# Kernel tuning notes

Hardware: AMD Instinct MI355X
Metric: run time of the kernel (lower is better)

Reference implementation:

```python
import jax, jax.numpy as jnp
import numpy as np

DIM = 2560
N_HEAD = 32
HEAD_DIM = 80
ROT_DIM = 32  # head_dim * partial_rotary_factor
INTER = 10240
EPS = 1e-5
BASE = 10000.0


def setup_inputs() -> dict:
    key = jax.random.key(0)
    ks = jax.random.split(key, 12)
    B, S, D, I = 1, 2048, DIM, INTER
    s = lambda k, shape, scale: (jax.random.normal(k, shape, jnp.float32) * scale)
    return {
        "x": s(ks[0], (B, S, D), 1.0),
        "input_pos": jnp.arange(S, dtype=jnp.int32),
        "mask": jnp.tril(jnp.ones((S, S), dtype=bool)),
        "ln_w": jnp.ones((D,), jnp.float32),
        "ln_b": jnp.zeros((D,), jnp.float32),
        "wqkv_w": s(ks[1], (3 * D, D), 0.02),
        "wqkv_b": jnp.zeros((3 * D,), jnp.float32),
        "wo_w": s(ks[2], (D, D), 0.02),
        "wo_b": jnp.zeros((D,), jnp.float32),
        "w1_w": s(ks[3], (I, D), 0.02),
        "w1_b": jnp.zeros((I,), jnp.float32),
        "w2_w": s(ks[4], (D, I), 0.02),
        "w2_b": jnp.zeros((D,), jnp.float32),
    }


def _rope_cos_sin(positions):
    # positions: [S] int; returns cos,sin of shape [S, ROT_DIM]
    inv_freq = 1.0 / (BASE ** (jnp.arange(0, ROT_DIM, 2, dtype=jnp.float32) / ROT_DIM))
    freqs = positions.astype(jnp.float32)[:, None] * inv_freq[None, :]  # [S, ROT/2]
    emb = jnp.concatenate([freqs, freqs], axis=-1)  # [S, ROT]
    return jnp.cos(emb), jnp.sin(emb)


def _rotate_half(t):
    t1, t2 = jnp.split(t, 2, axis=-1)
    return jnp.concatenate([-t2, t1], axis=-1)


def _apply_rope(t, cos, sin):
    # t: [B,H,S,hd]; rotary applied to first ROT_DIM dims (partial rotary)
    t_rot, t_pass = t[..., :ROT_DIM], t[..., ROT_DIM:]
    t_rot = t_rot * cos[None, None] + _rotate_half(t_rot) * sin[None, None]
    return jnp.concatenate([t_rot, t_pass], axis=-1)


def reference(x, input_pos, mask, ln_w, ln_b, wqkv_w, wqkv_b, wo_w, wo_b,
              w1_w, w1_b, w2_w, w2_b):
    B, S, D = x.shape
    H, hd = N_HEAD, HEAD_DIM
    # shared LayerNorm (parallel block)
    mu = jnp.mean(x, axis=-1, keepdims=True)
    var = jnp.mean(jnp.square(x - mu), axis=-1, keepdims=True)
    h = (x - mu) * jax.lax.rsqrt(var + EPS) * ln_w + ln_b

    # fused QKV
    qkv = h @ wqkv_w.T + wqkv_b  # [B,S,3D]
    q, k, v = jnp.split(qkv, 3, axis=-1)
    q = q.reshape(B, S, H, hd).transpose(0, 2, 1, 3)  # [B,H,S,hd]
    k = k.reshape(B, S, H, hd).transpose(0, 2, 1, 3)
    v = v.reshape(B, S, H, hd).transpose(0, 2, 1, 3)

    cos, sin = _rope_cos_sin(input_pos)
    q = _apply_rope(q, cos, sin)
    k = _apply_rope(k, cos, sin)

    # causal attention
    scores = jnp.einsum("bhqd,bhkd->bhqk", q, k) / np.sqrt(hd).astype(np.float32)
    scores = jnp.where(mask[None, None], scores, jnp.float32(-1e9))
    attn = jax.nn.softmax(scores, axis=-1)
    y = jnp.einsum("bhqk,bhkd->bhqd", attn, v)  # [B,H,S,hd]
    y = y.transpose(0, 2, 1, 3).reshape(B, S, D)
    attn_out = y @ wo_w.T + wo_b

    # fused MLP (phi2: gelu_new / tanh approx)
    ffn = jax.nn.gelu(h @ w1_w.T + w1_b, approximate=True) @ w2_w.T + w2_b

    return attn_out + ffn + x
```

## Files before the change

kernel.cpp:

```cpp
#include <hip/hip_runtime.h>
#include <cstdint>

#define S_LEN 2048
#define DMODEL 2560
#define NHEADS 32
#define HDIM 80
#define DINTER 10240

typedef unsigned short u16;
typedef __bf16 bf16x8 __attribute__((ext_vector_type(8)));
typedef float f32x4 __attribute__((ext_vector_type(4)));

__device__ __forceinline__ float us2f(u16 u) {
  return __builtin_bit_cast(float, ((uint32_t)u) << 16);
}
__device__ __forceinline__ u16 f2us(float f) {
  uint32_t x = __builtin_bit_cast(uint32_t, f);
  x += 0x7fffu + ((x >> 16) & 1u);
  return (u16)(x >> 16);
}

typedef __attribute__((address_space(1))) void gas_void;
typedef __attribute__((address_space(3))) void las_void;
__device__ __forceinline__ void gld16(const void* g, void* l) {
  __builtin_amdgcn_global_load_lds((gas_void*)g, (las_void*)l, 16, 0, 0);
}

#define VMW(N) asm volatile("s_waitcnt vmcnt(" #N ")" ::: "memory")
#define BARRIER()                          \
  do {                                     \
    asm volatile("" ::: "memory");         \
    __builtin_amdgcn_s_barrier();          \
    asm volatile("" ::: "memory");         \
  } while (0)

__global__ void f2b_kernel(const float* __restrict__ src, u16* __restrict__ dst) {
  const size_t i = ((size_t)blockIdx.x * 256 + threadIdx.x) * 8;
  const float4 a = *(const float4*)(src + i);
  const float4 b = *(const float4*)(src + i + 4);
  u16 o[8] = {f2us(a.x), f2us(a.y), f2us(a.z), f2us(a.w),
              f2us(b.x), f2us(b.y), f2us(b.z), f2us(b.w)};
  *(uint4*)(dst + i) = *(uint4*)o;
}

__global__ void initout_kernel(const float* __restrict__ x,
                               const float* __restrict__ wo_b,
                               const float* __restrict__ w2_b,
                               float* __restrict__ out) {
  const size_t idx = ((size_t)blockIdx.x * 256 + threadIdx.x) * 4;
  const int c0 = (int)(idx % DMODEL);
  const float4 vx = *(const float4*)(x + idx);
  const float4 b1 = *(const float4*)(wo_b + c0);
  const float4 b2 = *(const float4*)(w2_b + c0);
  float4 vo;
  vo.x = vx.x + b1.x + b2.x;
  vo.y = vx.y + b1.y + b2.y;
  vo.z = vx.z + b1.z + b2.z;
  vo.w = vx.w + b1.w + b2.w;
  *(float4*)(out + idx) = vo;
}

__global__ void ln_kernel(const float* __restrict__ x, const float* __restrict__ w,
                          const float* __restrict__ b, u16* __restrict__ h) {
  const int s = blockIdx.x, tid = threadIdx.x;
  const float* xr = x + (size_t)s * DMODEL;
  float v[10];
  float sum = 0.f, sq = 0.f;
#pragma unroll
  for (int j = 0; j < 10; j++) {
    v[j] = xr[tid + j * 256];
    sum += v[j];
    sq += v[j] * v[j];
  }
#pragma unroll
  for (int o = 32; o > 0; o >>= 1) {
    sum += __shfl_down(sum, o, 64);
    sq += __shfl_down(sq, o, 64);
  }
  __shared__ float red[8];
  const int wave = tid >> 6, lane = tid & 63;
  if (lane == 0) { red[wave] = sum; red[4 + wave] = sq; }
  __syncthreads();
  sum = red[0] + red[1] + red[2] + red[3];
  sq = red[4] + red[5] + red[6] + red[7];
  const float mu = sum * (1.0f / DMODEL);
  const float var = sq * (1.0f / DMODEL) - mu * mu;
  const float rstd = rsqrtf(var + 1e-5f);
  u16* hr = h + (size_t)s * DMODEL;
#pragma unroll
  for (int j = 0; j < 10; j++) {
    const int d = tid + j * 256;
    hr[d] = f2us((v[j] - mu) * rstd * w[d] + b[d]);
  }
}

template <int ACT, int MODE>
__launch_bounds__(512, 2)
__global__ void gemm256(const u16* __restrict__ A, const u16* __restrict__ B,
                        const float* __restrict__ bias, void* __restrict__ Cv,
                        int M, int N, int K) {
  __shared__ __align__(16) u16 lds[3][16384];
  const int tid = threadIdx.x;
  const int w = tid >> 6, lane = tid & 63;
  const int quad = lane >> 4, l15 = lane & 15;
  const int wm = w >> 2, wn = w & 3;

  const int nwg = gridDim.x * gridDim.y;
  const int flat = blockIdx.x + gridDim.x * blockIdx.y;
  const int swz = (flat & 7) * (nwg >> 3) + (flat >> 3);
  const int ntN = N >> 8;
  const int bm = swz / ntN, bn = swz % ntN;

  const int Kc = K / gridDim.z;
  const int k0 = Kc * blockIdx.z;
  const int nt = Kc >> 5;

  const int g = ((lane & 3) ^ ((lane >> 3) & 3)) * 8;
  const u16* Ag = A + ((size_t)bm * 256 + w * 32 + (lane >> 2)) * K + k0 + g;
  const u16* Bg = B + ((size_t)bn * 256 + w * 32 + (lane >> 2)) * K + k0 + g;
  const size_t k16 = (size_t)16 * K;
  const int aw = w * 1024;

  const int rswz = (quad ^ ((l15 >> 1) & 3)) * 8;
  const int arow = wm * 128 + l15;
  const int brow = wn * 64 + l15;

#define STG(T)                                                               \
  do {                                                                       \
    const int q_ = (T) % 3;                                                  \
    const size_t ko_ = (size_t)(T) * 32;                                     \
    gld16(Ag + ko_, &lds[q_][aw]);                                           \
    gld16(Ag + ko_ + k16, &lds[q_][aw + 512]);                               \
    gld16(Bg + ko_, &lds[q_][8192 + aw]);                                    \
    gld16(Bg + ko_ + k16, &lds[q_][8192 + aw + 512]);                        \
  } while (0)

#define TILE_BODY(T)                                                         \
  do {                                                                       \
    const int qb_ = (T) % 3;                                                 \
    bf16x8 aF[8], bF[4];                                                     \
    _Pragma("unroll") for (int mf_ = 0; mf_ < 8; mf_++)                      \
        aF[mf_] = *(const bf16x8*)&lds[qb_][(arow + mf_ * 16) * 32 + rswz];  \
    _Pragma("unroll") for (int nf_ = 0; nf_ < 4; nf_++)                      \
        bF[nf_] = *(const bf16x8*)&lds[qb_][8192 + (brow + nf_ * 16) * 32 + rswz]; \
    __builtin_amdgcn_s_setprio(1);                                           \
    _Pragma("unroll") for (int mf_ = 0; mf_ < 8; mf_++)                      \
    _Pragma("unroll") for (int nf_ = 0; nf_ < 4; nf_++)                      \
        acc[mf_][nf_] = __builtin_amdgcn_mfma_f32_16x16x32_bf16(             \
            aF[mf_], bF[nf_], acc[mf_][nf_], 0, 0, 0);                       \
    __builtin_amdgcn_s_setprio(0);                                           \
  } while (0)

  f32x4 acc[8][4] = {};

  STG(0);
  STG(1);

  for (int t = 0; t < nt - 1; ++t) {
    VMW(4);
    BARRIER();
    if (t + 2 < nt) STG(t + 2);
    TILE_BODY(t);
  }
  {
    VMW(0);
    BARRIER();
    TILE_BODY(nt - 1);
  }

#pragma unroll
  for (int nf = 0; nf < 4; nf++) {
    const int col = bn * 256 + wn * 64 + nf * 16 + l15;
    const float bv = (MODE == 0) ? bias[col] : 0.f;
#pragma unroll
    for (int mf = 0; mf < 8; mf++) {
      const int row0 = bm * 256 + wm * 128 + mf * 16 + quad * 4;
#pragma unroll
      for (int r = 0; r < 4; r++) {
        float v = acc[mf][nf][r] + bv;
        if (ACT == 1) {
          const float tt = v * (0.7978845608f + 0.0356774081f * v * v);
          v = 0.5f * v * (1.0f + tanhf(tt));
        }
        if (MODE == 0)
          ((u16*)Cv)[(size_t)(row0 + r) * N + col] = f2us(v);
        else
          atomicAdd((float*)Cv + (size_t)(row0 + r) * N + col, v);
      }
    }
  }
#undef STG
#undef TILE_BODY
}

__global__ void rope_kernel(u16* __restrict__ qkv, const int* __restrict__ pos) {
  const int idx = blockIdx.x * 256 + threadIdx.x;
  const int i = idx & 15;
  const int which = (idx >> 4) & 1;
  const int hh = (idx >> 5) & 31;
  const int s = idx >> 10;
  const float p = (float)pos[s];
  const float freq = p * expf(-0.57564627324851f * (float)i);
  float sn, c;
  sincosf(freq, &sn, &c);
  u16* base = qkv + (size_t)s * (3 * DMODEL) + which * DMODEL + hh * HDIM + i;
  const float t0 = us2f(base[0]), t1 = us2f(base[16]);
  base[0] = f2us(t0 * c - t1 * sn);
  base[16] = f2us(t1 * c + t0 * sn);
}

__global__ void attn_kernel(const u16* __restrict__ qkv, u16* __restrict__ y) {
  const int qt = (int)gridDim.x - 1 - (int)blockIdx.x;
  const int h = blockIdx.y;
  const int tid = threadIdx.x, wave = tid >> 6, lane = tid & 63;
  const int quad = lane >> 4, l15 = lane & 15;
  const int qbase = qt * 64;

  __shared__ __align__(16) u16 Qs[64 * 104];
  __shared__ __align__(16) u16 Ks[2][64 * 104];
  __shared__ __align__(16) u16 Vts[2][80 * 88];
  __shared__ __align__(16) u16 Ps[4][2][16 * 40];

  if (tid < 128) {
    const int b = tid >> 6, r = tid & 63;
    u16* z = &Ks[b][r * 104 + 80];
    *(uint4*)z = uint4{0, 0, 0, 0};
    *(uint4*)(z + 8) = uint4{0, 0, 0, 0};
  } else if (tid < 192) {
    const int r = tid & 63;
    u16* z = &Qs[r * 104 + 80];
    *(uint4*)z = uint4{0, 0, 0, 0};
    *(uint4*)(z + 8) = uint4{0, 0, 0, 0};
    *(uint4*)(z + 16) = uint4{0, 0, 0, 0};
  }

  {
    const int r = tid >> 2, c = tid & 3;
    const u16* src = qkv + (size_t)(qbase + r) * (3 * DMODEL) + h * HDIM + c * 20;
    u16* dst = Qs + r * 104 + c * 20;
#pragma unroll
    for (int j = 0; j < 5; j++) {
      ushort4 uv = *(const ushort4*)(src + j * 4);
      ushort4 ov;
      ov.x = f2us(us2f(uv.x) * 0.11180339887f);
      ov.y = f2us(us2f(uv.y) * 0.11180339887f);
      ov.z = f2us(us2f(uv.z) * 0.11180339887f);
      ov.w = f2us(us2f(uv.w) * 0.11180339887f);
      *(ushort4*)(dst + j * 4) = ov;
    }
  }

  {
    const int r = tid >> 2, c4 = (tid & 3) * 20;
    const u16* sK = qkv + (size_t)r * (3 * DMODEL) + DMODEL + h * HDIM + c4;
    u16* dK = &Ks[0][r * 104 + c4];
#pragma unroll
    for (int j = 0; j < 5; j++) *(uint2*)(dK + j * 4) = *(const uint2*)(sK + j * 4);
  }
  if (tid < 160) {
    const int p = tid & 31, cc = tid >> 5;
    const u16* sV = qkv + (size_t)(2 * p) * (3 * DMODEL) + 2 * DMODEL + h * HDIM + cc * 16;
    const uint4 a0 = *(const uint4*)sV;
    const uint4 b0 = *(const uint4*)(sV + 8);
    const uint4 a1 = *(const uint4*)(sV + 3 * DMODEL);
    const uint4 b1 = *(const uint4*)(sV + 3 * DMODEL + 8);
    const uint32_t A0[8] = {a0.x, a0.y, a0.z, a0.w, b0.x, b0.y, b0.z, b0.w};
    const uint32_t A1[8] = {a1.x, a1.y, a1.z, a1.w, b1.x, b1.y, b1.z, b1.w};
    uint32_t* dV = (uint32_t*)Vts[0];
#pragma unroll
    for (int d = 0; d < 16; d++) {
      const int j = d >> 1, s = (d & 1) * 16;
      const uint32_t o = ((A0[j] >> s) & 0xffffu) | (((A1[j] >> s) & 0xffffu) << 16);
      dV[(cc * 16 + d) * 44 + p] = o;
    }
  }

  float m_i[4], l_i[4];
  f32x4 oacc[5] = {};
#pragma unroll
  for (int r = 0; r < 4; r++) { m_i[r] = -1e30f; l_i[r] = 0.f; }

  __syncthreads();

  bf16x8 aq[3];
#pragma unroll
  for (int ks = 0; ks < 3; ks++)
    aq[ks] = *(const bf16x8*)&Qs[(wave * 16 + l15) * 104 + ks * 32 + quad * 8];

  const int n_iter = qt + 1;
  uint2 kr[5];
  uint4 v0a = {}, v0b = {}, v1a = {}, v1b = {};

  for (int it = 0; it < n_iter; ++it) {
    const int cur = it & 1;
    const bool more = (it + 1 < n_iter);
    if (more) {
      const int kcn = (it + 1) * 64;
      const int r = tid >> 2, c4 = (tid & 3) * 20;
      const u16* sK = qkv + (size_t)(kcn + r) * (3 * DMODEL) + DMODEL + h * HDIM + c4;
#pragma unroll
      for (int j = 0; j < 5; j++) kr[j] = *(const uint2*)(sK + j * 4);
      if (tid < 160) {
        const int p = tid & 31, cc = tid >> 5;
        const u16* sV =
            qkv + (size_t)(kcn + 2 * p) * (3 * DMODEL) + 2 * DMODEL + h * HDIM + cc * 16;
        v0a = *(const uint4*)sV;
        v0b = *(const uint4*)(sV + 8);
        v1a = *(const uint4*)(sV + 3 * DMODEL);
        v1b = *(const uint4*)(sV + 3 * DMODEL + 8);
      }
    }

    const int kc0 = it * 64;
    f32x4 st[4] = {};
#pragma unroll
    for (int ks = 0; ks < 3; ks++)
#pragma unroll
      for (int t = 0; t < 4; t++) {
        bf16x8 bk = *(const bf16x8*)&Ks[cur][(t * 16 + l15) * 104 + ks * 32 + quad * 8];
        st[t] = __builtin_amdgcn_mfma_f32_16x16x32_bf16(aq[ks], bk, st[t], 0, 0, 0);
      }

    float sv[4][4], mx[4];
    if (it == qt) {
#pragma unroll
      for (int r = 0; r < 4; r++) {
        const int qr = qbase + wave * 16 + quad * 4 + r;
#pragma unroll
        for (int t = 0; t < 4; t++) {
          const int kc = kc0 + t * 16 + l15;
          sv[t][r] = (kc <= qr) ? st[t][r] : -1e30f;
        }
      }
    } else {
#pragma unroll
      for (int r = 0; r < 4; r++)
#pragma unroll
        for (int t = 0; t < 4; t++) sv[t][r] = st[t][r];
    }
#pragma unroll
    for (int r = 0; r < 4; r++)
      mx[r] = fmaxf(fmaxf(sv[0][r], sv[1][r]), fmaxf(sv[2][r], sv[3][r]));
#pragma unroll
    for (int o = 1; o < 16; o <<= 1)
#pragma unroll
      for (int r = 0; r < 4; r++) mx[r] = fmaxf(mx[r], __shfl_xor(mx[r], o, 64));

    float alpha[4], rs[4];
#pragma unroll
    for (int r = 0; r < 4; r++) {
      const float mnew = fmaxf(m_i[r], mx[r]);
      alpha[r] = __expf(m_i[r] - mnew);
      m_i[r] = mnew;
      const float p0 = __expf(sv[0][r] - mnew);
      const float p1 = __expf(sv[1][r] - mnew);
      const float p2 = __expf(sv[2][r] - mnew);
      const float p3 = __expf(sv[3][r] - mnew);
      rs[r] = (p0 + p1) + (p2 + p3);
      const int ro = (quad * 4 + r) * 40;
      Ps[wave][0][ro + l15] = f2us(p0);
      Ps[wave][0][ro + 16 + l15] = f2us(p1);
      Ps[wave][1][ro + l15] = f2us(p2);
      Ps[wave][1][ro + 16 + l15] = f2us(p3);
    }
#pragma unroll
    for (int o = 1; o < 16; o <<= 1)
#pragma unroll
      for (int r = 0; r < 4; r++) rs[r] += __shfl_xor(rs[r], o, 64);
#pragma unroll
    for (int r = 0; r < 4; r++) l_i[r] = l_i[r] * alpha[r] + rs[r];
#pragma unroll
    for (int dt = 0; dt < 5; dt++)
#pragma unroll
      for (int r = 0; r < 4; r++) oacc[dt][r] *= alpha[r];

    bf16x8 pf0 = *(const bf16x8*)&Ps[wave][0][l15 * 40 + quad * 8];
    bf16x8 pf1 = *(const bf16x8*)&Ps[wave][1][l15 * 40 + quad * 8];
#pragma unroll
    for (int dt = 0; dt < 5; dt++) {
      bf16x8 vf0 = *(const bf16x8*)&Vts[cur][(dt * 16 + l15) * 88 + quad * 8];
      bf16x8 vf1 = *(const bf16x8*)&Vts[cur][(dt * 16 + l15) * 88 + 32 + quad * 8];
      oacc[dt] = __builtin_amdgcn_mfma_f32_16x16x32_bf16(pf0, vf0, oacc[dt], 0, 0, 0);
      oacc[dt] = __builtin_amdgcn_mfma_f32_16x16x32_bf16(pf1, vf1, oacc[dt], 0, 0, 0);
    }

    if (more) {
      const int r = tid >> 2, c4 = (tid & 3) * 20;
      u16* dK = &Ks[cur ^ 1][r * 104 + c4];
#pragma unroll
      for (int j = 0; j < 5; j++) *(uint2*)(dK + j * 4) = kr[j];
      if (tid < 160) {
        const int p = tid & 31, cc = tid >> 5;
        const uint32_t A0[8] = {v0a.x, v0a.y, v0a.z, v0a.w,
                                v0b.x, v0b.y, v0b.z, v0b.w};
        const uint32_t A1[8] = {v1a.x, v1a.y, v1a.z, v1a.w,
                                v1b.x, v1b.y, v1b.z, v1b.w};
        uint32_t* dV = (uint32_t*)Vts[cur ^ 1];
#pragma unroll
        for (int d = 0; d < 16; d++) {
          const int j = d >> 1, s = (d & 1) * 16;
          const uint32_t o =
              ((A0[j] >> s) & 0xffffu) | (((A1[j] >> s) & 0xffffu) << 16);
          dV[(cc * 16 + d) * 44 + p] = o;
        }
      }
    }
    __syncthreads();
  }

#pragma unroll
  for (int dt = 0; dt < 5; dt++)
#pragma unroll
    for (int r = 0; r < 4; r++) {
      const int row = qbase + wave * 16 + quad * 4 + r;
      y[(size_t)row * DMODEL + h * HDIM + dt * 16 + l15] = f2us(oacc[dt][r] / l_i[r]);
    }
}

extern "C" void kernel_launch(void* const* d_in, const int* in_sizes, int n_in,
                              void* d_out, int out_size, void* d_ws, size_t ws_size,
                              hipStream_t stream) {
  const float* x = (const float*)d_in[0];
  const int* pos = (const int*)d_in[1];
  const float* ln_w = (const float*)d_in[3];
  const float* ln_b = (const float*)d_in[4];
  const float* wqkv_w = (const float*)d_in[5];
  const float* wqkv_b = (const float*)d_in[6];
  const float* wo_w = (const float*)d_in[7];
  const float* wo_b = (const float*)d_in[8];
  const float* w1_w = (const float*)d_in[9];
  const float* w1_b = (const float*)d_in[10];
  const float* w2_w = (const float*)d_in[11];
  const float* w2_b = (const float*)d_in[12];
  float* out = (float*)d_out;

  char* ws = (char*)d_ws;
  u16* wbuf = (u16*)(ws);
  u16* h = (u16*)(ws + 52428800);
  u16* ffn1 = (u16*)(ws + 62914560);
  u16* qkv = (u16*)(ws + 62914560);
  u16* yAtt = (u16*)(ws + 94371840);

  ln_kernel<<<S_LEN, 256, 0, stream>>>(x, ln_w, ln_b, h);
  initout_kernel<<<(S_LEN * DMODEL / 4) / 256, 256, 0, stream>>>(x, wo_b, w2_b, out);

  f2b_kernel<<<(DINTER * DMODEL) / 2048, 256, 0, stream>>>(w1_w, wbuf);
  gemm256<1, 0><<<dim3(DINTER / 256, S_LEN / 256, 1), 512, 0, stream>>>(
      h, wbuf, w1_b, ffn1, S_LEN, DINTER, DMODEL);
  f2b_kernel<<<(DMODEL * DINTER) / 2048, 256, 0, stream>>>(w2_w, wbuf);
  gemm256<0, 2><<<dim3(DMODEL / 256, S_LEN / 256, 5), 512, 0, stream>>>(
      ffn1, wbuf, w2_b, out, S_LEN, DMODEL, DINTER);

  f2b_kernel<<<(3 * DMODEL * DMODEL) / 2048, 256, 0, stream>>>(wqkv_w, wbuf);
  gemm256<0, 0><<<dim3(3 * DMODEL / 256, S_LEN / 256, 1), 512, 0, stream>>>(
      h, wbuf, wqkv_b, qkv, S_LEN, 3 * DMODEL, DMODEL);
  rope_kernel<<<(S_LEN * NHEADS * 2 * 16) / 256, 256, 0, stream>>>(qkv, pos);
  attn_kernel<<<dim3(S_LEN / 64, NHEADS), 256, 0, stream>>>(qkv, yAtt);
  f2b_kernel<<<(DMODEL * DMODEL) / 2048, 256, 0, stream>>>(wo_w, wbuf);
  gemm256<0, 2><<<dim3(DMODEL / 256, S_LEN / 256, 2), 512, 0, stream>>>(
      yAtt, wbuf, wo_b, out, S_LEN, DMODEL, DMODEL);
}
```

Baseline: 1.036 ms.

## Replace 256x256 triple-buffered GEMM with 128x128 single-buffered GEMM

Swaps the 256x256-tile, 512-thread GEMM, which uses a three-stage LDS ring with async prefetch, for a 128x128-tile, 256-thread kernel with one LDS buffer that loads, waits, and computes each K step in turn. Launch grids are resized to match, and the w2 split-K factor drops from 5 to 4. Smaller tiles give more workgroups and lower LDS use per block, which could help occupancy and tail balance. In exchange, the global-to-LDS prefetch overlap is lost and each tile reuses data less, so global traffic rises.

```diff
diff --git a/kernel.cpp b/kernel.cpp
--- a/kernel.cpp
+++ b/kernel.cpp
@@ -95,20 +95,21 @@
 }
 
 template <int ACT, int MODE>
-__launch_bounds__(512, 2)
-__global__ void gemm256(const u16* __restrict__ A, const u16* __restrict__ B,
+__launch_bounds__(256, 3)
+__global__ void gemm128(const u16* __restrict__ A, const u16* __restrict__ B,
                         const float* __restrict__ bias, void* __restrict__ Cv,
                         int M, int N, int K) {
-  __shared__ __align__(16) u16 lds[3][16384];
+  __shared__ __align__(16) u16 As[128 * 32];
+  __shared__ __align__(16) u16 Bs[128 * 32];
   const int tid = threadIdx.x;
   const int w = tid >> 6, lane = tid & 63;
   const int quad = lane >> 4, l15 = lane & 15;
-  const int wm = w >> 2, wn = w & 3;
+  const int wm = w >> 1, wn = w & 1;
 
   const int nwg = gridDim.x * gridDim.y;
   const int flat = blockIdx.x + gridDim.x * blockIdx.y;
   const int swz = (flat & 7) * (nwg >> 3) + (flat >> 3);
-  const int ntN = N >> 8;
+  const int ntN = N >> 7;
   const int bm = swz / ntN, bn = swz % ntN;
 
   const int Kc = K / gridDim.z;
@@ -116,65 +117,50 @@
   const int nt = Kc >> 5;
 
   const int g = ((lane & 3) ^ ((lane >> 3) & 3)) * 8;
-  const u16* Ag = A + ((size_t)bm * 256 + w * 32 + (lane >> 2)) * K + k0 + g;
-  const u16* Bg = B + ((size_t)bn * 256 + w * 32 + (lane >> 2)) * K + k0 + g;
+  const u16* Ag = A + ((size_t)bm * 128 + w * 32 + (lane >> 2)) * K + k0 + g;
+  const u16* Bg = B + ((size_t)bn * 128 + w * 32 + (lane >> 2)) * K + k0 + g;
   const size_t k16 = (size_t)16 * K;
   const int aw = w * 1024;
 
   const int rswz = (quad ^ ((l15 >> 1) & 3)) * 8;
-  const int arow = wm * 128 + l15;
+  const int arow = wm * 64 + l15;
   const int brow = wn * 64 + l15;
 
-#define STG(T)                                                               \
-  do {                                                                       \
-    const int q_ = (T) % 3;                                                  \
-    const size_t ko_ = (size_t)(T) * 32;                                     \
-    gld16(Ag + ko_, &lds[q_][aw]);                                           \
-    gld16(Ag + ko_ + k16, &lds[q_][aw + 512]);                               \
-    gld16(Bg + ko_, &lds[q_][8192 + aw]);                                    \
-    gld16(Bg + ko_ + k16, &lds[q_][8192 + aw + 512]);                        \
-  } while (0)
-
-#define TILE_BODY(T)                                                         \
-  do {                                                                       \
-    const int qb_ = (T) % 3;                                                 \
-    bf16x8 aF[8], bF[4];                                                     \
-    _Pragma("unroll") for (int mf_ = 0; mf_ < 8; mf_++)                      \
-        aF[mf_] = *(const bf16x8*)&lds[qb_][(arow + mf_ * 16) * 32 + rswz];  \
-    _Pragma("unroll") for (int nf_ = 0; nf_ < 4; nf_++)                      \
-        bF[nf_] = *(const bf16x8*)&lds[qb_][8192 + (brow + nf_ * 16) * 32 + rswz]; \
-    __builtin_amdgcn_s_setprio(1);                                           \
-    _Pragma("unroll") for (int mf_ = 0; mf_ < 8; mf_++)                      \
-    _Pragma("unroll") for (int nf_ = 0; nf_ < 4; nf_++)                      \
-        acc[mf_][nf_] = __builtin_amdgcn_mfma_f32_16x16x32_bf16(             \
-            aF[mf_], bF[nf_], acc[mf_][nf_], 0, 0, 0);                       \
-    __builtin_amdgcn_s_setprio(0);                                           \
-  } while (0)
-
-  f32x4 acc[8][4] = {};
-
-  STG(0);
-  STG(1);
-
-  for (int t = 0; t < nt - 1; ++t) {
-    VMW(4);
-    BARRIER();
-    if (t + 2 < nt) STG(t + 2);
-    TILE_BODY(t);
-  }
-  {
+  f32x4 acc[4][4] = {};
+
+  for (int t = 0; t < nt; ++t) {
+    const size_t ko = (size_t)t * 32;
+    gld16(Ag + ko, &As[aw]);
+    gld16(Ag + ko + k16, &As[aw + 512]);
+    gld16(Bg + ko, &Bs[aw]);
+    gld16(Bg + ko + k16, &Bs[aw + 512]);
     VMW(0);
     BARRIER();
-    TILE_BODY(nt - 1);
+    bf16x8 aF[4], bF[4];
+#pragma unroll
+    for (int mf = 0; mf < 4; mf++)
+      aF[mf] = *(const bf16x8*)&As[(arow + mf * 16) * 32 + rswz];
+#pragma unroll
+    for (int nf = 0; nf < 4; nf++)
+      bF[nf] = *(const bf16x8*)&Bs[(brow + nf * 16) * 32 + rswz];
+    __builtin_amdgcn_s_setprio(1);
+#pragma unroll
+    for (int mf = 0; mf < 4; mf++)
+#pragma unroll
+      for (int nf = 0; nf < 4; nf++)
+        acc[mf][nf] = __builtin_amdgcn_mfma_f32_16x16x32_bf16(
+            aF[mf], bF[nf], acc[mf][nf], 0, 0, 0);
+    __builtin_amdgcn_s_setprio(0);
+    BARRIER();
   }
 
 #pragma unroll
   for (int nf = 0; nf < 4; nf++) {
-    const int col = bn * 256 + wn * 64 + nf * 16 + l15;
+    const int col = bn * 128 + wn * 64 + nf * 16 + l15;
     const float bv = (MODE == 0) ? bias[col] : 0.f;
 #pragma unroll
-    for (int mf = 0; mf < 8; mf++) {
-      const int row0 = bm * 256 + wm * 128 + mf * 16 + quad * 4;
+    for (int mf = 0; mf < 4; mf++) {
+      const int row0 = bm * 128 + wm * 64 + mf * 16 + quad * 4;
 #pragma unroll
       for (int r = 0; r < 4; r++) {
         float v = acc[mf][nf][r] + bv;
@@ -189,8 +175,6 @@
       }
     }
   }
-#undef STG
-#undef TILE_BODY
 }
 
 __global__ void rope_kernel(u16* __restrict__ qkv, const int* __restrict__ pos) {
@@ -445,18 +429,18 @@
   initout_kernel<<<(S_LEN * DMODEL / 4) / 256, 256, 0, stream>>>(x, wo_b, w2_b, out);
 
   f2b_kernel<<<(DINTER * DMODEL) / 2048, 256, 0, stream>>>(w1_w, wbuf);
-  gemm256<1, 0><<<dim3(DINTER / 256, S_LEN / 256, 1), 512, 0, stream>>>(
+  gemm128<1, 0><<<dim3(DINTER / 128, S_LEN / 128, 1), 256, 0, stream>>>(
       h, wbuf, w1_b, ffn1, S_LEN, DINTER, DMODEL);
   f2b_kernel<<<(DMODEL * DINTER) / 2048, 256, 0, stream>>>(w2_w, wbuf);
-  gemm256<0, 2><<<dim3(DMODEL / 256, S_LEN / 256, 5), 512, 0, stream>>>(
+  gemm128<0, 2><<<dim3(DMODEL / 128, S_LEN / 128, 4), 256, 0, stream>>>(
       ffn1, wbuf, w2_b, out, S_LEN, DMODEL, DINTER);
 
   f2b_kernel<<<(3 * DMODEL * DMODEL) / 2048, 256, 0, stream>>>(wqkv_w, wbuf);
-  gemm256<0, 0><<<dim3(3 * DMODEL / 256, S_LEN / 256, 1), 512, 0, stream>>>(
+  gemm128<0, 0><<<dim3(3 * DMODEL / 128, S_LEN / 128, 1), 256, 0, stream>>>(
       h, wbuf, wqkv_b, qkv, S_LEN, 3 * DMODEL, DMODEL);
   rope_kernel<<<(S_LEN * NHEADS * 2 * 16) / 256, 256, 0, stream>>>(qkv, pos);
   attn_kernel<<<dim3(S_LEN / 64, NHEADS), 256, 0, stream>>>(qkv, yAtt);
   f2b_kernel<<<(DMODEL * DMODEL) / 2048, 256, 0, stream>>>(wo_w, wbuf);
-  gemm256<0, 2><<<dim3(DMODEL / 256, S_LEN / 256, 2), 512, 0, stream>>>(
+  gemm128<0, 2><<<dim3(DMODEL / 128, S_LEN / 128, 2), 256, 0, stream>>>(
       yAtt, wbuf, wo_b, out, S_LEN, DMODEL, DMODEL);
 }
```

Result: faster. 1.009 ms (-2.7%).
